# Kernel optimization log

Measured on AMD Instinct MI355X. Metric: run time of the kernel, lower is better.

Reference implementation:

```python
import jax, jax.numpy as jnp
import numpy as np
from jax import lax

B, C, H, W, E = 16, 256, 64, 64, 4
KH = KW = 3
EPS = 1e-5  # torch BatchNorm2d default


def conv2d(x, w, groups=1):
    # x: [N, Cin, H, W], w: [Cout, Cin/groups, KH, KW], stride 1, pad 1 (autopad for k=3)
    return lax.conv_general_dilated(
        x, w, window_strides=(1, 1), padding=[(1, 1), (1, 1)],
        dimension_numbers=('NCHW', 'OIHW', 'NCHW'),
        feature_group_count=groups)


def bn(t, g, b, m, v):
    # eval-mode batchnorm over channel dim of [N, C, H, W]
    scale = g / jnp.sqrt(v + EPS)
    return (t - m[:, None, None]) * scale[:, None, None] + b[:, None, None]


def silu(t):
    return t * jax.nn.sigmoid(t)


def setup_inputs() -> dict:
    key = jax.random.key(0)
    ks = jax.random.split(key, 8)
    s = lambda k, sh: jax.random.normal(k, sh, jnp.float32) * 0.05
    return {
        'x': jax.random.normal(ks[0], (B, C, H, W), jnp.float32),
        # cv1: Conv(c1, c_, 3) = conv(no bias) + BN + SiLU
        'w1': s(ks[1], (C, C, KH, KW)),
        'bn1_g': jnp.ones((C,), jnp.float32),
        'bn1_b': jnp.zeros((C,), jnp.float32),
        'bn1_m': s(ks[2], (C,)),
        'bn1_v': jnp.abs(s(ks[3], (C,))) + 1.0,
        # cv2: DynamicConv routing linear (C -> E experts)
        'wr': s(ks[4], (E, C)),
        'br': jnp.zeros((E,), jnp.float32),
        # CondConv2d expert weight bank: [E, Cout*Cin*KH*KW]
        'w_e': s(ks[5], (E, C * C * KH * KW)),
        # cv2 BatchNorm2d
        'bn2_g': jnp.ones((C,), jnp.float32),
        'bn2_b': jnp.zeros((C,), jnp.float32),
        'bn2_m': s(ks[6], (C,)),
        'bn2_v': jnp.abs(s(ks[7], (C,))) + 1.0,
    }


def reference(x, w1, bn1_g, bn1_b, bn1_m, bn1_v, wr, br, w_e,
              bn2_g, bn2_b, bn2_m, bn2_v):
    # cv1: standard YOLO Conv (3x3, pad 1) + BN + SiLU
    y = silu(bn(conv2d(x, w1), bn1_g, bn1_b, bn1_m, bn1_v))  # [B, C, H, W]

    # DynamicConv_Single: global-avg-pool routing -> sigmoid gates over experts
    pooled = y.mean(axis=(2, 3))                       # [B, C]
    routing = jax.nn.sigmoid(pooled @ wr.T + br)       # [B, E]

    # CondConv2d: per-sample expert-weighted kernel, applied via batch-as-groups
    kern = (routing @ w_e).reshape(B * C, C, KH, KW)   # [B*Cout, Cin, 3, 3]
    yc = conv2d(y.reshape(1, B * C, H, W), kern, groups=B).reshape(B, C, H, W)

    # cv2 BN + SiLU, then residual add (shortcut and c1 == c2)
    out = silu(bn(yc, bn2_g, bn2_b, bn2_m, bn2_v))
    return x + out


if __name__ == '__main__':
    o = reference(**setup_inputs())
    print(o.shape, o.dtype)
```

## Files before the change

### kernel.cpp

```cpp
#include <hip/hip_runtime.h>
#include <math.h>

typedef _Float16 h16;
typedef _Float16 half8 __attribute__((ext_vector_type(8)));
typedef float f32x4 __attribute__((ext_vector_type(4)));

#define BATCH 16
#define CH 256
#define EPSBN 1e-5f

constexpr size_t WE_STRIDE = (size_t)CH * CH * 9;
constexpr int REG = 2120;

__device__ __forceinline__ float silu_(float v) {
    return v * (1.0f / (1.0f + __expf(-v)));
}

template<int MODE>
__global__ __launch_bounds__(256, 4)
void conv_mfma(const h16* __restrict__ xin,
               const h16* __restrict__ wt,
               const float* __restrict__ bng, const float* __restrict__ bnb,
               const float* __restrict__ bnm, const float* __restrict__ bnv,
               const float* __restrict__ resid,
               void* __restrict__ outv)
{
    __shared__ h16 xt[4 * REG];

    const int t = threadIdx.x;
    const int swz = (blockIdx.x & 7) * 128 + (blockIdx.x >> 3);
    const int bx  = swz & 31;
    const int gy  = swz >> 5;
    const int by  = gy & 1;
    const int bz  = gy >> 1;
    const int h0  = bx * 2;
    const int co0 = by * 128;
    const int wv   = t >> 6;
    const int ws   = wv >> 1;
    const int wc   = wv & 1;
    const int lane = t & 63;
    const int quad = lane >> 4;
    const int l15  = lane & 15;

    f32x4 acc[16];
    #pragma unroll
    for (int i = 0; i < 16; ++i) {
        f32x4 z = {0.f, 0.f, 0.f, 0.f};
        acc[i] = z;
    }

    const h16* wrow = wt + ((MODE == 1) ? (size_t)bz * 9 * 65536 : (size_t)0)
                         + ((size_t)(co0 + wc * 64 + l15) << 8)
                         + (size_t)(quad * 8);

    const h16* xb = xin + ((size_t)bz << 20);
    int goff[5], lofs[5];
    #pragma unroll
    for (int k = 0; k < 5; ++k) {
        int idx = t + k * 256;
        goff[k] = -1;
        lofs[k] = -1;
        if (idx < 1056) {
            int cig = idx & 3;
            int sp  = idx >> 2;
            int row = sp / 66;
            int col = sp - row * 66;
            int gh = h0 - 1 + row, gw = col - 1;
            lofs[k] = cig * REG + sp * 8;
            if ((unsigned)gh < 64u && (unsigned)gw < 64u)
                goff[k] = ((gh << 6) + gw) * 256 + cig * 8;
        }
    }

    const h16* xlane = xt + quad * REG + l15 * 8;

    for (int c = 0; c < 8; ++c) {
        const int ci0 = c * 32;
        __syncthreads();
        #pragma unroll
        for (int k = 0; k < 5; ++k) {
            if (lofs[k] >= 0) {
                half8 v = {0, 0, 0, 0, 0, 0, 0, 0};
                if (goff[k] >= 0) v = *(const half8*)(xb + goff[k] + ci0);
                *(half8*)(xt + lofs[k]) = v;
            }
        }
        __syncthreads();

        const h16* wcp = wrow + ci0;
        #pragma unroll
        for (int kh = 0; kh < 3; ++kh)
        #pragma unroll
        for (int kw = 0; kw < 3; ++kw) {
            const int tap = kh * 3 + kw;
            half8 wf[4], xf[4];
            #pragma unroll
            for (int f = 0; f < 4; ++f)
                wf[f] = *(const half8*)(wcp + (size_t)tap * 65536 + f * 4096);
            #pragma unroll
            for (int i = 0; i < 4; ++i)
                xf[i] = *(const half8*)(xlane + ((ws + kh) * 66 + i * 16 + kw) * 8);
            if (MODE == 0) {
                #pragma unroll
                for (int i = 0; i < 4; ++i)
                    #pragma unroll
                    for (int j = 0; j < 4; ++j)
                        acc[i * 4 + j] = __builtin_amdgcn_mfma_f32_16x16x32_f16(
                            xf[i], wf[j], acc[i * 4 + j], 0, 0, 0);
            } else {
                #pragma unroll
                for (int i = 0; i < 4; ++i)
                    #pragma unroll
                    for (int j = 0; j < 4; ++j)
                        acc[i * 4 + j] = __builtin_amdgcn_mfma_f32_16x16x32_f16(
                            wf[i], xf[j], acc[i * 4 + j], 0, 0, 0);
            }
        }
    }

    if (MODE == 0) {
        h16* yout = (h16*)outv;
        float sc[4], sh[4];
        #pragma unroll
        for (int j = 0; j < 4; ++j) {
            int cch = co0 + wc * 64 + j * 16 + l15;
            float s = bng[cch] * rsqrtf(bnv[cch] + EPSBN);
            sc[j] = s; sh[j] = bnb[cch] - bnm[cch] * s;
        }
        const int h = h0 + ws;
        #pragma unroll
        for (int i = 0; i < 4; ++i)
            #pragma unroll
            for (int r = 0; r < 4; ++r) {
                int w = i * 16 + quad * 4 + r;
                size_t base = (((size_t)(bz * 64 + h) << 6) + w) * 256
                            + co0 + wc * 64 + l15;
                #pragma unroll
                for (int j = 0; j < 4; ++j) {
                    float v = acc[i * 4 + j][r] * sc[j] + sh[j];
                    yout[base + j * 16] = (h16)silu_(v);
                }
            }
    } else {
        float* outp = (float*)outv;
        const int h = h0 + ws;
        #pragma unroll
        for (int i = 0; i < 4; ++i) {
            float sc[4], sh[4];
            #pragma unroll
            for (int r = 0; r < 4; ++r) {
                int cch = co0 + wc * 64 + i * 16 + quad * 4 + r;
                float s = bng[cch] * rsqrtf(bnv[cch] + EPSBN);
                sc[r] = s; sh[r] = bnb[cch] - bnm[cch] * s;
            }
            #pragma unroll
            for (int j = 0; j < 4; ++j) {
                int w = j * 16 + l15;
                #pragma unroll
                for (int r = 0; r < 4; ++r) {
                    int cch = co0 + wc * 64 + i * 16 + quad * 4 + r;
                    size_t idx = ((size_t)(bz * CH + cch) << 12) + (h << 6) + w;
                    float v = acc[i * 4 + j][r] * sc[r] + sh[r];
                    outp[idx] = resid[idx] + silu_(v);
                }
            }
        }
    }
}

__global__ __launch_bounds__(256)
void prep_x(const float* __restrict__ x, h16* __restrict__ xh) {
    __shared__ float lt[64][65];
    int cg = blockIdx.x, h = blockIdx.y, b = blockIdx.z;
    int t = threadIdx.x;
    {
        int cl = t >> 2, wq = t & 3;
        const float4* src = (const float4*)(x + (((size_t)(b * CH + cg * 64 + cl)) << 12)
                                              + ((size_t)h << 6));
        #pragma unroll
        for (int k = 0; k < 4; ++k) {
            int w4 = wq + k * 4;
            float4 v = src[w4];
            lt[cl][w4 * 4 + 0] = v.x;
            lt[cl][w4 * 4 + 1] = v.y;
            lt[cl][w4 * 4 + 2] = v.z;
            lt[cl][w4 * 4 + 3] = v.w;
        }
    }
    __syncthreads();
    {
        int wl = t >> 2, cq = t & 3;
        half8 a2[2];
        h16* ap = (h16*)a2;
        #pragma unroll
        for (int m = 0; m < 16; ++m) ap[m] = (h16)lt[cq * 16 + m][wl];
        size_t base = ((((size_t)(b * 64 + h)) << 6) + wl) * 256 + cg * 64 + cq * 16;
        *(half8*)(xh + base)     = a2[0];
        *(half8*)(xh + base + 8) = a2[1];
    }
}

__global__ void prep_w1(const float* __restrict__ w1, h16* __restrict__ w1t) {
    int pair = blockIdx.x * 256 + threadIdx.x;
    #pragma unroll
    for (int tap = 0; tap < 9; ++tap)
        w1t[((size_t)tap << 16) + pair] = (h16)w1[(size_t)pair * 9 + tap];
}

__global__ __launch_bounds__(256)
void pool_kernel(const h16* __restrict__ y, float* __restrict__ part) {
    __shared__ float red[8][256];
    int slice = blockIdx.x, b = blockIdx.y;
    int t = threadIdx.x;
    int oct = t & 31, ss = t >> 5;
    float a[8];
    #pragma unroll
    for (int k = 0; k < 8; ++k) a[k] = 0.f;
    const h16* p = y + ((size_t)(b * 4096 + slice * 256 + ss)) * 256 + oct * 8;
    #pragma unroll 4
    for (int i = 0; i < 32; ++i) {
        half8 v = *(const half8*)(p + (size_t)i * 8 * 256);
        #pragma unroll
        for (int k = 0; k < 8; ++k) a[k] += (float)v[k];
    }
    #pragma unroll
    for (int k = 0; k < 8; ++k) red[ss][oct * 8 + k] = a[k];
    __syncthreads();
    float s = 0.f;
    #pragma unroll
    for (int q = 0; q < 8; ++q) s += red[q][t];
    part[((size_t)slice * BATCH + b) * 256 + t] = s;
}

__global__ void routing_kernel(const float* __restrict__ part,
                               const float* __restrict__ wr,
                               const float* __restrict__ br,
                               float* __restrict__ routing) {
    int t = threadIdx.x;
    if (t < 64) {
        int b = t >> 2, e = t & 3;
        float s = 0.f;
        for (int c = 0; c < 256; ++c) {
            float p = 0.f;
            for (int sl = 0; sl < 16; ++sl)
                p += part[((size_t)sl * BATCH + b) * 256 + c];
            s += p * wr[e * 256 + c];
        }
        s = s * (1.f / 4096.f) + br[e];
        routing[t] = 1.f / (1.f + __expf(-s));
    }
}

__global__ __launch_bounds__(256)
void kern_gen(const float* __restrict__ w_e,
              const float* __restrict__ routing,
              h16* __restrict__ wt2) {
    __shared__ float lw[4 * 2304];
    __shared__ float rsh[64];
    int t = threadIdx.x;
    int pair0 = blockIdx.x * 256;
    if (t < 64) rsh[t] = routing[t];
    #pragma unroll
    for (int e = 0; e < 4; ++e) {
        const float4* src = (const float4*)(w_e + (size_t)e * WE_STRIDE + (size_t)pair0 * 9);
        #pragma unroll
        for (int k = 0; k < 3; ++k) {
            int idx = t + k * 256;
            if (idx < 576) {
                float4 v = src[idx];
                float* d = &lw[e * 2304 + idx * 4];
                d[0] = v.x; d[1] = v.y; d[2] = v.z; d[3] = v.w;
            }
        }
    }
    __syncthreads();
    float wv[4][9];
    #pragma unroll
    for (int e = 0; e < 4; ++e)
        #pragma unroll
        for (int k = 0; k < 9; ++k)
            wv[e][k] = lw[e * 2304 + t * 9 + k];
    for (int b = 0; b < 16; ++b) {
        float r0 = rsh[b * 4 + 0], r1 = rsh[b * 4 + 1];
        float r2 = rsh[b * 4 + 2], r3 = rsh[b * 4 + 3];
        #pragma unroll
        for (int tap = 0; tap < 9; ++tap) {
            float s = r0 * wv[0][tap] + r1 * wv[1][tap]
                    + r2 * wv[2][tap] + r3 * wv[3][tap];
            wt2[((size_t)(b * 9 + tap) << 16) + pair0 + t] = (h16)s;
        }
    }
}

extern "C" void kernel_launch(void* const* d_in, const int* in_sizes, int n_in,
                              void* d_out, int out_size, void* d_ws, size_t ws_size,
                              hipStream_t stream) {
    const float* x    = (const float*)d_in[0];
    const float* w1   = (const float*)d_in[1];
    const float* bn1g = (const float*)d_in[2];
    const float* bn1b = (const float*)d_in[3];
    const float* bn1m = (const float*)d_in[4];
    const float* bn1v = (const float*)d_in[5];
    const float* wr   = (const float*)d_in[6];
    const float* br   = (const float*)d_in[7];
    const float* w_e  = (const float*)d_in[8];
    const float* bn2g = (const float*)d_in[9];
    const float* bn2b = (const float*)d_in[10];
    const float* bn2m = (const float*)d_in[11];
    const float* bn2v = (const float*)d_in[12];

    char* w = (char*)d_ws;
    h16*   xh      = (h16*)(w);
    h16*   y       = (h16*)(w + 33554432);
    h16*   w1t     = (h16*)(w + 67108864);
    h16*   wt2     = (h16*)(w + 68288512);
    float* part    = (float*)(w + 87162880);
    float* routing = (float*)(w + 87425024);

    prep_x<<<dim3(4, 64, BATCH), 256, 0, stream>>>(x, xh);
    prep_w1<<<dim3(256), 256, 0, stream>>>(w1, w1t);

    dim3 cgrid(1024);
    conv_mfma<0><<<cgrid, 256, 0, stream>>>(xh, w1t, bn1g, bn1b, bn1m, bn1v,
                                            nullptr, y);
    pool_kernel<<<dim3(16, BATCH), 256, 0, stream>>>(y, part);
    routing_kernel<<<dim3(1), 64, 0, stream>>>(part, wr, br, routing);
    kern_gen<<<dim3(256), 256, 0, stream>>>(w_e, routing, wt2);
    conv_mfma<1><<<cgrid, 256, 0, stream>>>(y, wt2, bn2g, bn2b, bn2m, bn2v,
                                            x, (float*)d_out);
}
```

Measured before the change: 533.8 us.

## Stage conv weights in LDS and retile blocks to 4 rows by 64 channels

The conv kernel now stages each 32-channel weight slice for all 9 taps into shared memory, so waves read weight fragments from LDS instead of each fetching them from global memory. The block tile changes from 2 output rows by 128 output channels to 4 rows by 64 channels, with each wave owning one row and all 64 channels, and the input halo grows to 6 rows. This cuts redundant global weight traffic and reuses each weight across more spatial rows. The cost is more LDS per block and a lower occupancy hint (2 instead of 4 blocks), which may hurt latency hiding.

```diff
diff --git a/kernel.cpp b/kernel.cpp
--- a/kernel.cpp
+++ b/kernel.cpp
@@ -10,14 +10,15 @@
 #define EPSBN 1e-5f
 
 constexpr size_t WE_STRIDE = (size_t)CH * CH * 9;
-constexpr int REG = 2120;
+constexpr int XREG = 3176;
+constexpr int WREG = 292;
 
 __device__ __forceinline__ float silu_(float v) {
     return v * (1.0f / (1.0f + __expf(-v)));
 }
 
 template<int MODE>
-__global__ __launch_bounds__(256, 4)
+__global__ __launch_bounds__(256, 2)
 void conv_mfma(const h16* __restrict__ xin,
                const h16* __restrict__ wt,
                const float* __restrict__ bng, const float* __restrict__ bnb,
@@ -25,19 +26,18 @@
                const float* __restrict__ resid,
                void* __restrict__ outv)
 {
-    __shared__ h16 xt[4 * REG];
+    __shared__ h16 xt[4 * XREG];
+    __shared__ h16 wlds[64 * WREG];
 
     const int t = threadIdx.x;
     const int swz = (blockIdx.x & 7) * 128 + (blockIdx.x >> 3);
-    const int bx  = swz & 31;
-    const int gy  = swz >> 5;
-    const int by  = gy & 1;
-    const int bz  = gy >> 1;
-    const int h0  = bx * 2;
-    const int co0 = by * 128;
-    const int wv   = t >> 6;
-    const int ws   = wv >> 1;
-    const int wc   = wv & 1;
+    const int bx  = swz & 15;
+    const int gy  = swz >> 4;
+    const int by  = gy & 3;
+    const int bz  = gy >> 2;
+    const int h0  = bx * 4;
+    const int co0 = by * 64;
+    const int ws   = t >> 6;
     const int lane = t & 63;
     const int quad = lane >> 4;
     const int l15  = lane & 15;
@@ -49,36 +49,44 @@
         acc[i] = z;
     }
 
-    const h16* wrow = wt + ((MODE == 1) ? (size_t)bz * 9 * 65536 : (size_t)0)
-                         + ((size_t)(co0 + wc * 64 + l15) << 8)
-                         + (size_t)(quad * 8);
+    const h16* wbase = wt + ((MODE == 1) ? (size_t)bz * 9 * 65536 : (size_t)0);
+    const int wgoff = (co0 + (t >> 2)) * 256 + (t & 3) * 8;
+    const int wlofs = (t >> 2) * WREG + (t & 3) * 8;
 
     const h16* xb = xin + ((size_t)bz << 20);
-    int goff[5], lofs[5];
-    #pragma unroll
-    for (int k = 0; k < 5; ++k) {
+    int goff[7], lofs[7];
+    #pragma unroll
+    for (int k = 0; k < 7; ++k) {
         int idx = t + k * 256;
         goff[k] = -1;
         lofs[k] = -1;
-        if (idx < 1056) {
+        if (idx < 1584) {
             int cig = idx & 3;
             int sp  = idx >> 2;
             int row = sp / 66;
             int col = sp - row * 66;
             int gh = h0 - 1 + row, gw = col - 1;
-            lofs[k] = cig * REG + sp * 8;
+            lofs[k] = cig * XREG + sp * 8;
             if ((unsigned)gh < 64u && (unsigned)gw < 64u)
                 goff[k] = ((gh << 6) + gw) * 256 + cig * 8;
         }
     }
 
-    const h16* xlane = xt + quad * REG + l15 * 8;
+    const h16* xq = xt + quad * XREG + l15 * 8;
+    const h16* wq = wlds + l15 * WREG + quad * 8;
 
     for (int c = 0; c < 8; ++c) {
         const int ci0 = c * 32;
         __syncthreads();
-        #pragma unroll
-        for (int k = 0; k < 5; ++k) {
+        {
+            const h16* wg = wbase + wgoff + ci0;
+            h16* wl = wlds + wlofs;
+            #pragma unroll
+            for (int k = 0; k < 9; ++k)
+                *(half8*)(wl + k * 32) = *(const half8*)(wg + (size_t)k * 65536);
+        }
+        #pragma unroll
+        for (int k = 0; k < 7; ++k) {
             if (lofs[k] >= 0) {
                 half8 v = {0, 0, 0, 0, 0, 0, 0, 0};
                 if (goff[k] >= 0) v = *(const half8*)(xb + goff[k] + ci0);
@@ -87,7 +95,6 @@
         }
         __syncthreads();
 
-        const h16* wcp = wrow + ci0;
         #pragma unroll
         for (int kh = 0; kh < 3; ++kh)
         #pragma unroll
@@ -96,10 +103,10 @@
             half8 wf[4], xf[4];
             #pragma unroll
             for (int f = 0; f < 4; ++f)
-                wf[f] = *(const half8*)(wcp + (size_t)tap * 65536 + f * 4096);
+                wf[f] = *(const half8*)(wq + f * 16 * WREG + tap * 32);
             #pragma unroll
             for (int i = 0; i < 4; ++i)
-                xf[i] = *(const half8*)(xlane + ((ws + kh) * 66 + i * 16 + kw) * 8);
+                xf[i] = *(const half8*)(xq + ((ws + kh) * 66 + i * 16 + kw) * 8);
             if (MODE == 0) {
                 #pragma unroll
                 for (int i = 0; i < 4; ++i)
@@ -123,7 +130,7 @@
         float sc[4], sh[4];
         #pragma unroll
         for (int j = 0; j < 4; ++j) {
-            int cch = co0 + wc * 64 + j * 16 + l15;
+            int cch = co0 + j * 16 + l15;
             float s = bng[cch] * rsqrtf(bnv[cch] + EPSBN);
             sc[j] = s; sh[j] = bnb[cch] - bnm[cch] * s;
         }
@@ -134,7 +141,7 @@
             for (int r = 0; r < 4; ++r) {
                 int w = i * 16 + quad * 4 + r;
                 size_t base = (((size_t)(bz * 64 + h) << 6) + w) * 256
-                            + co0 + wc * 64 + l15;
+                            + co0 + l15;
                 #pragma unroll
                 for (int j = 0; j < 4; ++j) {
                     float v = acc[i * 4 + j][r] * sc[j] + sh[j];
@@ -149,7 +156,7 @@
             float sc[4], sh[4];
             #pragma unroll
             for (int r = 0; r < 4; ++r) {
-                int cch = co0 + wc * 64 + i * 16 + quad * 4 + r;
+                int cch = co0 + i * 16 + quad * 4 + r;
                 float s = bng[cch] * rsqrtf(bnv[cch] + EPSBN);
                 sc[r] = s; sh[r] = bnb[cch] - bnm[cch] * s;
             }
@@ -158,7 +165,7 @@
                 int w = j * 16 + l15;
                 #pragma unroll
                 for (int r = 0; r < 4; ++r) {
-                    int cch = co0 + wc * 64 + i * 16 + quad * 4 + r;
+                    int cch = co0 + i * 16 + quad * 4 + r;
                     size_t idx = ((size_t)(bz * CH + cch) << 12) + (h << 6) + w;
                     float v = acc[i * 4 + j][r] * sc[r] + sh[r];
                     outp[idx] = resid[idx] + silu_(v);
```

After: 599.8 us. 12.4% more time.

## Double-buffer input tile in LDS using direct global_load_lds prefetch

Applied to the files above, without the earlier changes.

Replaces the synchronous register-staged copy of the input halo tile into shared memory with asynchronous global_load_lds transfers into a double buffer. The next channel chunk is prefetched while MFMAs run on the current one, and padding zeros are written once up front. This cuts one barrier per iteration and aims to hide global-load latency, at the cost of doubled LDS use, which may reduce occupancy. Nothing waits explicitly for the async loads before the barrier, so correctness depends on the compiler inserting vmcnt waits.

```diff
diff --git a/kernel.cpp b/kernel.cpp
--- a/kernel.cpp
+++ b/kernel.cpp
@@ -10,7 +10,8 @@
 #define EPSBN 1e-5f
 
 constexpr size_t WE_STRIDE = (size_t)CH * CH * 9;
-constexpr int REG = 2120;
+constexpr int RSTRIDE = 2120;
+constexpr int BUFH    = 4 * RSTRIDE;
 
 __device__ __forceinline__ float silu_(float v) {
     return v * (1.0f / (1.0f + __expf(-v)));
@@ -25,7 +26,7 @@
                const float* __restrict__ resid,
                void* __restrict__ outv)
 {
-    __shared__ h16 xt[4 * REG];
+    __shared__ h16 xt[2 * BUFH];
 
     const int t = threadIdx.x;
     const int swz = (blockIdx.x & 7) * 128 + (blockIdx.x >> 3);
@@ -54,40 +55,50 @@
                          + (size_t)(quad * 8);
 
     const h16* xb = xin + ((size_t)bz << 20);
-    int goff[5], lofs[5];
+    int goff[5];
     #pragma unroll
     for (int k = 0; k < 5; ++k) {
-        int idx = t + k * 256;
+        int slot = k * 64 + lane;
+        int row = slot / 66;
+        int col = slot - row * 66;
+        int gh = h0 - 1 + row, gw = col - 1;
         goff[k] = -1;
-        lofs[k] = -1;
-        if (idx < 1056) {
-            int cig = idx & 3;
-            int sp  = idx >> 2;
-            int row = sp / 66;
-            int col = sp - row * 66;
-            int gh = h0 - 1 + row, gw = col - 1;
-            lofs[k] = cig * REG + sp * 8;
-            if ((unsigned)gh < 64u && (unsigned)gw < 64u)
-                goff[k] = ((gh << 6) + gw) * 256 + cig * 8;
-        }
-    }
-
-    const h16* xlane = xt + quad * REG + l15 * 8;
+        if (slot < 264 && (unsigned)gh < 64u && (unsigned)gw < 64u)
+            goff[k] = ((gh << 6) + gw) * 256 + wv * 8;
+    }
+
+    {
+        half8 z = {0, 0, 0, 0, 0, 0, 0, 0};
+        #pragma unroll
+        for (int k = 0; k < 5; ++k) {
+            int slot = k * 64 + lane;
+            if (slot < 264 && goff[k] < 0) {
+                *(half8*)(xt + wv * RSTRIDE + slot * 8) = z;
+                *(half8*)(xt + BUFH + wv * RSTRIDE + slot * 8) = z;
+            }
+        }
+    }
+
+    auto stage = [&](int b, int ci0) {
+        const h16* g = xb + ci0;
+        #pragma unroll
+        for (int k = 0; k < 5; ++k) {
+            if (goff[k] >= 0)
+                __builtin_amdgcn_global_load_lds(
+                    (const __attribute__((address_space(1))) void*)(g + goff[k]),
+                    (__attribute__((address_space(3))) void*)(xt + b * BUFH + wv * RSTRIDE + k * 512),
+                    16, 0, 0);
+        }
+    };
+
+    stage(0, 0);
+    __syncthreads();
 
     for (int c = 0; c < 8; ++c) {
-        const int ci0 = c * 32;
-        __syncthreads();
-        #pragma unroll
-        for (int k = 0; k < 5; ++k) {
-            if (lofs[k] >= 0) {
-                half8 v = {0, 0, 0, 0, 0, 0, 0, 0};
-                if (goff[k] >= 0) v = *(const half8*)(xb + goff[k] + ci0);
-                *(half8*)(xt + lofs[k]) = v;
-            }
-        }
-        __syncthreads();
-
-        const h16* wcp = wrow + ci0;
+        if (c < 7) stage((c + 1) & 1, (c + 1) * 32);
+
+        const h16* xq  = xt + (c & 1) * BUFH + quad * RSTRIDE + l15 * 8;
+        const h16* wcp = wrow + c * 32;
         #pragma unroll
         for (int kh = 0; kh < 3; ++kh)
         #pragma unroll
@@ -99,7 +110,7 @@
                 wf[f] = *(const half8*)(wcp + (size_t)tap * 65536 + f * 4096);
             #pragma unroll
             for (int i = 0; i < 4; ++i)
-                xf[i] = *(const half8*)(xlane + ((ws + kh) * 66 + i * 16 + kw) * 8);
+                xf[i] = *(const half8*)(xq + ((ws + kh) * 66 + i * 16 + kw) * 8);
             if (MODE == 0) {
                 #pragma unroll
                 for (int i = 0; i < 4; ++i)
@@ -116,6 +127,7 @@
                             wf[i], xf[j], acc[i * 4 + j], 0, 0, 0);
             }
         }
+        __syncthreads();
     }
 
     if (MODE == 0) {
```

Measured after the change: 553.0 us. +3.6%, slower.
